# Optimization experiments

Measured on AMD Instinct MI355X. Metric: run time of the kernel, lower is better.

## Reference

```python
import jax, jax.numpy as jnp
import numpy as np
import math

jax.config.update("jax_enable_x64", True)

# cfg constants
N = 4096
DIM = 16
SA = 2.0        # sigma_a
SR = 0.5        # sigma_r
V_SCALE = 1.0
R_H = 6.0
TAU_H = 0.5
K0_KUR = 0.05
TAU_KUR = 2.0
EPS = 1e-7      # acosh clamp epsilon (K=1 curvature)
D_MIN = 0.08    # distance floor in pairwise_dist


def setup_inputs() -> dict:
    key = jax.random.key(0)
    d_star = SA * SR / (SA - SR) * math.log(SA / SR)
    r_init = 0.5 * d_star
    hs = jax.random.normal(key, (N, DIM), dtype=jnp.float64) * r_init
    ht = jnp.sqrt(1.0 + jnp.sum(hs ** 2, axis=-1, keepdims=True))
    h = jnp.concatenate([ht, hs], axis=-1)  # [N, DIM+1] on the hyperboloid
    return {"h": h}


def reference(h):
    """Pairwise hyperbolic distance -> LJ coupling K_geo -> Lorentz-log force F,
    plus LJ potential energy E. Matmul form: no [N,N,dim+1] intermediates."""
    n1 = h.shape[-1]
    metric = jnp.concatenate([-jnp.ones((1,), h.dtype), jnp.ones((n1 - 1,), h.dtype)])
    # Lorentz inner products for all pairs: [N, N] (fp64)
    inn = (h * metric) @ h.T
    # geodesic distance d = acosh(clamp(-<hi,hj>_L, 1+eps))  (K = 1)
    D = jnp.arccosh(jnp.clip(-inn, 1.0 + EPS))
    eye = jnp.eye(N, dtype=h.dtype)
    # exact pairwise_dist semantics: zero diag, add D_MIN to off-diag entries < D_MIN
    D_pair = D * (1.0 - eye) + D_MIN * (((D < D_MIN) & (eye < 0.5)).astype(h.dtype))

    # _build_K in float32 (K_local == 1 since use_dyn_curv=False, learn_K=False)
    D_f = D_pair.astype(jnp.float32)
    eye32 = eye.astype(jnp.float32)
    D_eff = jnp.clip(D_f, 0.05)  # (D / sqrt(clamp(Ki*Kj,1e-4))).clamp(min=0.05) with K_local=1
    dVdd = jnp.exp(-D_eff / SR) / SR - jnp.exp(-D_eff / SA) / SA
    K_geo = -dVdd * V_SCALE * (1.0 - eye32)
    K_geo = K_geo * jax.nn.sigmoid((R_H - D_eff) / TAU_H)  # causal horizon
    K_kur = K0_KUR * jnp.exp(-D_f / TAU_KUR) * (1.0 - eye32)

    # _force: F_i = sum_j K_geo_ij * log_{h_i}(h_j)
    # log_x(y) = d / sqrt(<x,y>^2 - 1) * (y + <x,y> x)
    denom = jnp.sqrt(jnp.clip(inn ** 2 - 1.0, 1e-15))
    C = K_geo.astype(h.dtype) * D / denom  # [N, N]; diag is 0 since K_geo diag is 0
    F = C @ h + jnp.sum(C * inn, axis=-1, keepdims=True) * h  # [N, DIM+1]
    F_norm = jnp.clip(jnp.linalg.norm(F, axis=-1, keepdims=True), 1e-8)
    F = F * jnp.minimum(6.0 / F_norm, 1.0)

    # lj_potential energy on D_pair
    V = V_SCALE * (jnp.exp(-D_pair / SA) - jnp.exp(-D_pair / SR))
    E = jnp.sum(V * (1.0 - eye)) * 0.5
    return F, E
```

## Files before the change

kernel.cpp:

```cpp
#include <hip/hip_runtime.h>

#define NPTS 4096
#define DIMP 17
#define ROWP 20
#define RROW 21
#define JPB  256
#define NSLAB (NPTS / JPB)
#define NIB   (NPTS / 64)
#define EOFF  (NSLAB * DIMP * NPTS)
#define NEP   (NSLAB * NIB)
#define REDF  (448 * RROW)

typedef float v2f __attribute__((ext_vector_type(2)));
typedef float v4f __attribute__((ext_vector_type(4)));

__global__ __launch_bounds__(512) void hydra_pair_kernel(
    const float* __restrict__ h, float* __restrict__ ws,
    float* __restrict__ out, const int use_ws) {
    const int tid   = threadIdx.x;
    const int lane  = tid & 63;
    const int wid   = tid >> 6;
    const int i     = blockIdx.x * 64 + lane;
    const int jbase = blockIdx.y * JPB;

    __shared__ __align__(16) float lds[REDF + 16];

    for (int idx = tid; idx < JPB * DIMP; idx += 512) {
        const int j = idx / DIMP;
        const int k = idx - j * DIMP;
        lds[j * ROWP + k] = h[jbase * DIMP + idx];
    }

    v2f nhp[8];
    float nh16;
#pragma unroll
    for (int p = 0; p < 8; ++p) {
        const float s1 = (p == 0) ? 1.0f : -1.0f;
        nhp[p].x = s1 * h[i * DIMP + 2 * p];
        nhp[p].y = -h[i * DIMP + 2 * p + 1];
    }
    nh16 = -h[i * DIMP + 16];

    __syncthreads();

    v2f acp[8];
#pragma unroll
    for (int p = 0; p < 8; ++p) acp[p] = (v2f)(0.0f);
    float ac16 = 0.0f, sm = 0.0f, eacc = 0.0f;

    const float* rowp = lds + (wid * 32) * ROWP;
    for (int jj = 0; jj < 32; ++jj, rowp += ROWP) {
        const v4f a0 = ((const v4f*)rowp)[0];
        const v4f a1 = ((const v4f*)rowp)[1];
        const v4f a2 = ((const v4f*)rowp)[2];
        const v4f a3 = ((const v4f*)rowp)[3];
        const float a16 = rowp[16];

        v2f c0 = nhp[0] * a0.lo;
        v2f c1 = nhp[1] * a0.hi;
        c0 = __builtin_elementwise_fma(nhp[2], a1.lo, c0);
        c1 = __builtin_elementwise_fma(nhp[3], a1.hi, c1);
        c0 = __builtin_elementwise_fma(nhp[4], a2.lo, c0);
        c1 = __builtin_elementwise_fma(nhp[5], a2.hi, c1);
        c0 = __builtin_elementwise_fma(nhp[6], a3.lo, c0);
        c1 = __builtin_elementwise_fma(nhp[7], a3.hi, c1);
        const v2f cs = c0 + c1;
        const float m = fmaf(nh16, a16, cs.x + cs.y);

        const float ss = fmaxf(fmaf(m, m, -1.0f), 2e-7f);
        const float r  = __builtin_amdgcn_rsqf(ss);
        const float w  = ((m - 1.0f) - ss * r) + 1.0f;
        const float lg = __logf(w);
        const float t  = __builtin_amdgcn_sqrtf(w);
        const float u  = w * w;
        const float K  = fmaf(0.5f, t, -(u + u));
        const float C  = (K * r) * (-lg);
        eacc += (t - u);
        sm = fmaf(C, m, sm);

        const v2f Cs = {C, C};
        acp[0] = __builtin_elementwise_fma(Cs, a0.lo, acp[0]);
        acp[1] = __builtin_elementwise_fma(Cs, a0.hi, acp[1]);
        acp[2] = __builtin_elementwise_fma(Cs, a1.lo, acp[2]);
        acp[3] = __builtin_elementwise_fma(Cs, a1.hi, acp[3]);
        acp[4] = __builtin_elementwise_fma(Cs, a2.lo, acp[4]);
        acp[5] = __builtin_elementwise_fma(Cs, a2.hi, acp[5]);
        acp[6] = __builtin_elementwise_fma(Cs, a3.lo, acp[6]);
        acp[7] = __builtin_elementwise_fma(Cs, a3.hi, acp[7]);
        ac16 = fmaf(C, a16, ac16);
    }

    float ac[DIMP];
    ac[0] = fmaf(-sm, nhp[0].x, acp[0].x);
    ac[1] = fmaf( sm, nhp[0].y, acp[0].y);
#pragma unroll
    for (int p = 1; p < 8; ++p) {
        ac[2 * p]     = fmaf(sm, nhp[p].x, acp[p].x);
        ac[2 * p + 1] = fmaf(sm, nhp[p].y, acp[p].y);
    }
    ac[16] = fmaf(sm, nh16, ac16);

#pragma unroll
    for (int off = 32; off > 0; off >>= 1) eacc += __shfl_xor(eacc, off);

    __syncthreads();
    if (wid > 0) {
        float* dst = lds + ((wid - 1) * 64 + lane) * RROW;
#pragma unroll
        for (int k = 0; k < DIMP; ++k) dst[k] = ac[k];
        if (lane == 0) lds[REDF + wid] = eacc;
    }
    __syncthreads();

    if (wid == 0) {
        float esum = eacc;
#pragma unroll
        for (int q = 1; q < 8; ++q) esum += lds[REDF + q];
#pragma unroll
        for (int q = 0; q < 7; ++q) {
            const float* src = lds + (q * 64 + lane) * RROW;
#pragma unroll
            for (int k = 0; k < DIMP; ++k) ac[k] += src[k];
        }
        if (use_ws) {
            float* dst = ws + (size_t)blockIdx.y * (DIMP * NPTS) + i;
#pragma unroll
            for (int k = 0; k < DIMP; ++k) dst[k * NPTS] = ac[k];
            if (lane == 0) ws[EOFF + blockIdx.y * NIB + blockIdx.x] = esum;
        } else {
#pragma unroll
            for (int k = 0; k < DIMP; ++k) atomicAdd(&out[i * DIMP + k], ac[k]);
            if (lane == 0) atomicAdd(&out[NPTS * DIMP], esum);
        }
    }
}

__global__ __launch_bounds__(256) void hydra_finalize_kernel(
    const float* __restrict__ ws, float* __restrict__ out, const int use_ws) {
    const int tid  = threadIdx.x;
    const int lane = tid & 63;
    const int q    = tid >> 6;
    const int i    = blockIdx.x * 64 + lane;

    __shared__ __align__(16) float red[3 * 64 * RROW + 8];

    float v[DIMP];
#pragma unroll
    for (int k = 0; k < DIMP; ++k) v[k] = 0.0f;

    if (use_ws) {
#pragma unroll
        for (int ssl = 0; ssl < NSLAB / 4; ++ssl) {
            const int s = q * (NSLAB / 4) + ssl;
            const float* base = ws + (size_t)s * (DIMP * NPTS) + i;
#pragma unroll
            for (int k = 0; k < DIMP; ++k) v[k] += base[k * NPTS];
        }
        if (q > 0) {
            float* dst = red + ((q - 1) * 64 + lane) * RROW;
#pragma unroll
            for (int k = 0; k < DIMP; ++k) dst[k] = v[k];
        }
        __syncthreads();
        if (q == 0) {
#pragma unroll
            for (int qq = 0; qq < 3; ++qq) {
                const float* src = red + (qq * 64 + lane) * RROW;
#pragma unroll
                for (int k = 0; k < DIMP; ++k) v[k] += src[k];
            }
        }
    } else if (q == 0) {
#pragma unroll
        for (int k = 0; k < DIMP; ++k) v[k] = out[i * DIMP + k];
    }

    if (q == 0) {
        float ss = 0.0f;
#pragma unroll
        for (int k = 0; k < DIMP; ++k) ss = fmaf(v[k], v[k], ss);
        const float nrm   = sqrtf(ss);
        const float scale = fminf(6.0f / fmaxf(nrm, 1e-8f), 1.0f);
#pragma unroll
        for (int k = 0; k < DIMP; ++k) out[i * DIMP + k] = v[k] * scale;
    }

    if (blockIdx.x == 0) {
        if (use_ws) {
            float e = 0.0f;
#pragma unroll
            for (int t = 0; t < NEP / 256; ++t) e += ws[EOFF + tid + t * 256];
#pragma unroll
            for (int off = 32; off > 0; off >>= 1) e += __shfl_xor(e, off);
            __shared__ float es[4];
            if (lane == 0) es[q] = e;
            __syncthreads();
            if (tid == 0) out[NPTS * DIMP] = 0.5f * (es[0] + es[1] + es[2] + es[3]);
        } else {
            if (tid == 0) out[NPTS * DIMP] *= 0.5f;
        }
    }
}

extern "C" void kernel_launch(void* const* d_in, const int* in_sizes, int n_in,
                              void* d_out, int out_size, void* d_ws, size_t ws_size,
                              hipStream_t stream) {
    const float* h = (const float*)d_in[0];
    float* out = (float*)d_out;
    float* ws  = (float*)d_ws;

    const size_t need = (size_t)(EOFF + NEP) * sizeof(float);
    const int use_ws = (ws_size >= need) ? 1 : 0;
    if (!use_ws) {
        hipMemsetAsync(d_out, 0, (size_t)out_size * sizeof(float), stream);
    }

    dim3 grid(NIB, NSLAB);
    hydra_pair_kernel<<<grid, 512, 0, stream>>>(h, ws, out, use_ws);
    hydra_finalize_kernel<<<64, 256, 0, stream>>>(ws, out, use_ws);
}
```

Measured before the change: 36.76 us.

## Fuse finalize into pair kernel via last-block-done atomic counters

New measurement: 75.83 us. 2.06x slower.

```diff
diff --git a/kernel.cpp b/kernel.cpp
--- a/kernel.cpp
+++ b/kernel.cpp
@@ -7,8 +7,11 @@
 #define JPB  256
 #define NSLAB (NPTS / JPB)
 #define NIB   (NPTS / 64)
-#define EOFF  (NSLAB * DIMP * NPTS)
-#define NEP   (NSLAB * NIB)
+#define FPART (NSLAB * DIMP * NPTS)
+#define WSE   FPART
+#define CCNT  (FPART + 1)
+#define WCNT  (FPART + 65)
+#define CTRLB ((1 + NIB + 1) * 4)
 #define REDF  (448 * RROW)
 
 typedef float v2f __attribute__((ext_vector_type(2)));
@@ -24,12 +27,14 @@
     const int jbase = blockIdx.y * JPB;
 
     __shared__ __align__(16) float lds[REDF + 16];
+    __shared__ int flag;
 
     for (int idx = tid; idx < JPB * DIMP; idx += 512) {
         const int j = idx / DIMP;
         const int k = idx - j * DIMP;
         lds[j * ROWP + k] = h[jbase * DIMP + idx];
     }
+    if (tid == 0) flag = 0;
 
     v2f nhp[8];
     float nh16;
@@ -126,80 +131,81 @@
             float* dst = ws + (size_t)blockIdx.y * (DIMP * NPTS) + i;
 #pragma unroll
             for (int k = 0; k < DIMP; ++k) dst[k * NPTS] = ac[k];
-            if (lane == 0) ws[EOFF + blockIdx.y * NIB + blockIdx.x] = esum;
+            if (lane == 0) atomicAdd(&ws[WSE], esum);
+            __threadfence();
+            if (lane == 0) {
+                int* colcnt = (int*)(ws + CCNT);
+                const int old = atomicAdd(&colcnt[blockIdx.x], 1);
+                if (old == NSLAB - 1) flag = 1;
+            }
         } else {
 #pragma unroll
             for (int k = 0; k < DIMP; ++k) atomicAdd(&out[i * DIMP + k], ac[k]);
             if (lane == 0) atomicAdd(&out[NPTS * DIMP], esum);
         }
     }
-}
-
-__global__ __launch_bounds__(256) void hydra_finalize_kernel(
-    const float* __restrict__ ws, float* __restrict__ out, const int use_ws) {
-    const int tid  = threadIdx.x;
-    const int lane = tid & 63;
-    const int q    = tid >> 6;
-    const int i    = blockIdx.x * 64 + lane;
-
-    __shared__ __align__(16) float red[3 * 64 * RROW + 8];
-
-    float v[DIMP];
-#pragma unroll
-    for (int k = 0; k < DIMP; ++k) v[k] = 0.0f;
-
-    if (use_ws) {
-#pragma unroll
-        for (int ssl = 0; ssl < NSLAB / 4; ++ssl) {
-            const int s = q * (NSLAB / 4) + ssl;
+    __syncthreads();
+
+    if (use_ws && flag) {
+        float v[DIMP];
+#pragma unroll
+        for (int k = 0; k < DIMP; ++k) v[k] = 0.0f;
+#pragma unroll
+        for (int t2 = 0; t2 < 2; ++t2) {
+            const int s = 2 * wid + t2;
             const float* base = ws + (size_t)s * (DIMP * NPTS) + i;
 #pragma unroll
             for (int k = 0; k < DIMP; ++k) v[k] += base[k * NPTS];
         }
-        if (q > 0) {
-            float* dst = red + ((q - 1) * 64 + lane) * RROW;
+        if (wid > 0) {
+            float* dst = lds + ((wid - 1) * 64 + lane) * RROW;
 #pragma unroll
             for (int k = 0; k < DIMP; ++k) dst[k] = v[k];
         }
         __syncthreads();
-        if (q == 0) {
-#pragma unroll
-            for (int qq = 0; qq < 3; ++qq) {
-                const float* src = red + (qq * 64 + lane) * RROW;
+        if (wid == 0) {
+#pragma unroll
+            for (int q = 0; q < 7; ++q) {
+                const float* src = lds + (q * 64 + lane) * RROW;
 #pragma unroll
                 for (int k = 0; k < DIMP; ++k) v[k] += src[k];
             }
-        }
-    } else if (q == 0) {
-#pragma unroll
-        for (int k = 0; k < DIMP; ++k) v[k] = out[i * DIMP + k];
-    }
-
-    if (q == 0) {
-        float ss = 0.0f;
-#pragma unroll
-        for (int k = 0; k < DIMP; ++k) ss = fmaf(v[k], v[k], ss);
-        const float nrm   = sqrtf(ss);
+            float ssn = 0.0f;
+#pragma unroll
+            for (int k = 0; k < DIMP; ++k) ssn = fmaf(v[k], v[k], ssn);
+            const float nrm   = sqrtf(ssn);
+            const float scale = fminf(6.0f / fmaxf(nrm, 1e-8f), 1.0f);
+#pragma unroll
+            for (int k = 0; k < DIMP; ++k) out[i * DIMP + k] = v[k] * scale;
+        }
+        if (tid == 0) {
+            int* wincnt = (int*)(ws + WCNT);
+            const int old2 = atomicAdd(wincnt, 1);
+            if (old2 == NIB - 1) {
+                const float E = atomicAdd(&ws[WSE], 0.0f);
+                out[NPTS * DIMP] = 0.5f * E;
+            }
+        }
+    }
+}
+
+__global__ __launch_bounds__(256) void hydra_finalize_kernel(
+    float* __restrict__ out) {
+    const int i = blockIdx.x * 256 + threadIdx.x;
+    if (i < NPTS) {
+        float v[DIMP];
+        float ssn = 0.0f;
+#pragma unroll
+        for (int k = 0; k < DIMP; ++k) {
+            v[k] = out[i * DIMP + k];
+            ssn = fmaf(v[k], v[k], ssn);
+        }
+        const float nrm   = sqrtf(ssn);
         const float scale = fminf(6.0f / fmaxf(nrm, 1e-8f), 1.0f);
 #pragma unroll
         for (int k = 0; k < DIMP; ++k) out[i * DIMP + k] = v[k] * scale;
     }
-
-    if (blockIdx.x == 0) {
-        if (use_ws) {
-            float e = 0.0f;
-#pragma unroll
-            for (int t = 0; t < NEP / 256; ++t) e += ws[EOFF + tid + t * 256];
-#pragma unroll
-            for (int off = 32; off > 0; off >>= 1) e += __shfl_xor(e, off);
-            __shared__ float es[4];
-            if (lane == 0) es[q] = e;
-            __syncthreads();
-            if (tid == 0) out[NPTS * DIMP] = 0.5f * (es[0] + es[1] + es[2] + es[3]);
-        } else {
-            if (tid == 0) out[NPTS * DIMP] *= 0.5f;
-        }
-    }
+    if (blockIdx.x == 0 && threadIdx.x == 0) out[NPTS * DIMP] *= 0.5f;
 }
 
 extern "C" void kernel_launch(void* const* d_in, const int* in_sizes, int n_in,
@@ -209,13 +215,18 @@
     float* out = (float*)d_out;
     float* ws  = (float*)d_ws;
 
-    const size_t need = (size_t)(EOFF + NEP) * sizeof(float);
+    const size_t need = (size_t)(FPART + 66) * sizeof(float);
     const int use_ws = (ws_size >= need) ? 1 : 0;
-    if (!use_ws) {
+
+    if (use_ws) {
+        hipMemsetAsync(ws + WSE, 0, CTRLB, stream);
+    } else {
         hipMemsetAsync(d_out, 0, (size_t)out_size * sizeof(float), stream);
     }
 
     dim3 grid(NIB, NSLAB);
     hydra_pair_kernel<<<grid, 512, 0, stream>>>(h, ws, out, use_ws);
-    hydra_finalize_kernel<<<64, 256, 0, stream>>>(ws, out, use_ws);
+    if (!use_ws) {
+        hydra_finalize_kernel<<<NPTS / 256, 256, 0, stream>>>(out);
+    }
 }
```

## Broadcast j-rows via readlane from registers instead of LDS staging

Applied to the files above, without the earlier changes.

After: 49.54 us. 1.35x slower.

```diff
diff --git a/kernel.cpp b/kernel.cpp
--- a/kernel.cpp
+++ b/kernel.cpp
@@ -2,70 +2,56 @@
 
 #define NPTS 4096
 #define DIMP 17
-#define ROWP 20
 #define RROW 21
 #define JPB  256
 #define NSLAB (NPTS / JPB)
 #define NIB   (NPTS / 64)
 #define EOFF  (NSLAB * DIMP * NPTS)
 #define NEP   (NSLAB * NIB)
-#define REDF  (448 * RROW)
+#define REDF  (192 * RROW)
 
-typedef float v2f __attribute__((ext_vector_type(2)));
 typedef float v4f __attribute__((ext_vector_type(4)));
 
-__global__ __launch_bounds__(512) void hydra_pair_kernel(
+#define RL(x, l) __uint_as_float(__builtin_amdgcn_readlane(__float_as_uint(x), (l)))
+
+__global__ __launch_bounds__(256) void hydra_pair_kernel(
     const float* __restrict__ h, float* __restrict__ ws,
     float* __restrict__ out, const int use_ws) {
-    const int tid   = threadIdx.x;
-    const int lane  = tid & 63;
-    const int wid   = tid >> 6;
-    const int i     = blockIdx.x * 64 + lane;
-    const int jbase = blockIdx.y * JPB;
+    const int tid  = threadIdx.x;
+    const int lane = tid & 63;
+    const int wid  = tid >> 6;
+    const int i    = blockIdx.x * 64 + lane;
+    const int j0   = blockIdx.y * JPB + wid * 64;
 
-    __shared__ __align__(16) float lds[REDF + 16];
+    __shared__ float lds[REDF + 16];
 
-    for (int idx = tid; idx < JPB * DIMP; idx += 512) {
-        const int j = idx / DIMP;
-        const int k = idx - j * DIMP;
-        lds[j * ROWP + k] = h[jbase * DIMP + idx];
-    }
+    float hjr[DIMP];
+#pragma unroll
+    for (int k = 0; k < DIMP; ++k) hjr[k] = h[(j0 + lane) * DIMP + k];
 
-    v2f nhp[8];
-    float nh16;
+    float nh[DIMP];
 #pragma unroll
-    for (int p = 0; p < 8; ++p) {
-        const float s1 = (p == 0) ? 1.0f : -1.0f;
-        nhp[p].x = s1 * h[i * DIMP + 2 * p];
-        nhp[p].y = -h[i * DIMP + 2 * p + 1];
-    }
-    nh16 = -h[i * DIMP + 16];
+    for (int k = 0; k < DIMP; ++k) nh[k] = -h[i * DIMP + k];
+    nh[0] = -nh[0];
 
-    __syncthreads();
+    float ac[DIMP];
+#pragma unroll
+    for (int k = 0; k < DIMP; ++k) ac[k] = 0.0f;
+    float sm = 0.0f, eacc = 0.0f;
 
-    v2f acp[8];
+#pragma unroll 2
+    for (int jj = 0; jj < 64; ++jj) {
+        float b[DIMP];
 #pragma unroll
-    for (int p = 0; p < 8; ++p) acp[p] = (v2f)(0.0f);
-    float ac16 = 0.0f, sm = 0.0f, eacc = 0.0f;
+        for (int k = 0; k < DIMP; ++k) b[k] = RL(hjr[k], jj);
 
-    const float* rowp = lds + (wid * 32) * ROWP;
-    for (int jj = 0; jj < 32; ++jj, rowp += ROWP) {
-        const v4f a0 = ((const v4f*)rowp)[0];
-        const v4f a1 = ((const v4f*)rowp)[1];
-        const v4f a2 = ((const v4f*)rowp)[2];
-        const v4f a3 = ((const v4f*)rowp)[3];
-        const float a16 = rowp[16];
-
-        v2f c0 = nhp[0] * a0.lo;
-        v2f c1 = nhp[1] * a0.hi;
-        c0 = __builtin_elementwise_fma(nhp[2], a1.lo, c0);
-        c1 = __builtin_elementwise_fma(nhp[3], a1.hi, c1);
-        c0 = __builtin_elementwise_fma(nhp[4], a2.lo, c0);
-        c1 = __builtin_elementwise_fma(nhp[5], a2.hi, c1);
-        c0 = __builtin_elementwise_fma(nhp[6], a3.lo, c0);
-        c1 = __builtin_elementwise_fma(nhp[7], a3.hi, c1);
-        const v2f cs = c0 + c1;
-        const float m = fmaf(nh16, a16, cs.x + cs.y);
+        float p0 = nh[0] * b[0], p1 = nh[1] * b[1];
+#pragma unroll
+        for (int k = 2; k < 16; k += 2) {
+            p0 = fmaf(nh[k], b[k], p0);
+            p1 = fmaf(nh[k + 1], b[k + 1], p1);
+        }
+        const float m = fmaf(nh[16], b[16], p0 + p1);
 
         const float ss = fmaxf(fmaf(m, m, -1.0f), 2e-7f);
         const float r  = __builtin_amdgcn_rsqf(ss);
@@ -78,27 +64,13 @@
         eacc += (t - u);
         sm = fmaf(C, m, sm);
 
-        const v2f Cs = {C, C};
-        acp[0] = __builtin_elementwise_fma(Cs, a0.lo, acp[0]);
-        acp[1] = __builtin_elementwise_fma(Cs, a0.hi, acp[1]);
-        acp[2] = __builtin_elementwise_fma(Cs, a1.lo, acp[2]);
-        acp[3] = __builtin_elementwise_fma(Cs, a1.hi, acp[3]);
-        acp[4] = __builtin_elementwise_fma(Cs, a2.lo, acp[4]);
-        acp[5] = __builtin_elementwise_fma(Cs, a2.hi, acp[5]);
-        acp[6] = __builtin_elementwise_fma(Cs, a3.lo, acp[6]);
-        acp[7] = __builtin_elementwise_fma(Cs, a3.hi, acp[7]);
-        ac16 = fmaf(C, a16, ac16);
+#pragma unroll
+        for (int k = 0; k < DIMP; ++k) ac[k] = fmaf(C, b[k], ac[k]);
     }
 
-    float ac[DIMP];
-    ac[0] = fmaf(-sm, nhp[0].x, acp[0].x);
-    ac[1] = fmaf( sm, nhp[0].y, acp[0].y);
+    ac[0] = fmaf(-sm, nh[0], ac[0]);
 #pragma unroll
-    for (int p = 1; p < 8; ++p) {
-        ac[2 * p]     = fmaf(sm, nhp[p].x, acp[p].x);
-        ac[2 * p + 1] = fmaf(sm, nhp[p].y, acp[p].y);
-    }
-    ac[16] = fmaf(sm, nh16, ac16);
+    for (int k = 1; k < DIMP; ++k) ac[k] = fmaf(sm, nh[k], ac[k]);
 
 #pragma unroll
     for (int off = 32; off > 0; off >>= 1) eacc += __shfl_xor(eacc, off);
@@ -113,11 +85,9 @@
     __syncthreads();
 
     if (wid == 0) {
-        float esum = eacc;
+        const float esum = eacc + lds[REDF + 1] + lds[REDF + 2] + lds[REDF + 3];
 #pragma unroll
-        for (int q = 1; q < 8; ++q) esum += lds[REDF + q];
-#pragma unroll
-        for (int q = 0; q < 7; ++q) {
+        for (int q = 0; q < 3; ++q) {
             const float* src = lds + (q * 64 + lane) * RROW;
 #pragma unroll
             for (int k = 0; k < DIMP; ++k) ac[k] += src[k];
@@ -216,6 +186,6 @@
     }
 
     dim3 grid(NIB, NSLAB);
-    hydra_pair_kernel<<<grid, 512, 0, stream>>>(h, ws, out, use_ws);
+    hydra_pair_kernel<<<grid, 256, 0, stream>>>(h, ws, out, use_ws);
     hydra_finalize_kernel<<<64, 256, 0, stream>>>(ws, out, use_ws);
 }
```
